# Kernel tuning notes

Measured on AMD Instinct MI355X. Metric: run time of the kernel, lower is better.

## Reference

```python
import jax, jax.numpy as jnp
import numpy as np

B, C, H, W = 16, 64, 32, 32

def conv1x1(x, w, b=None):
    # x: [b,c,h,w], w: [o,c]
    y = jnp.einsum('bchw,oc->bohw', x, w)
    return y if b is None else y + b[None, :, None, None]

def bn(x, s, b, eps=1e-5):
    # training-mode batchnorm over (N,H,W)
    m = x.mean(axis=(0, 2, 3), keepdims=True)
    v = x.var(axis=(0, 2, 3), keepdims=True)
    return (x - m) * jax.lax.rsqrt(v + eps) * s[None, :, None, None] + b[None, :, None, None]

def block(x, w1, s1, b1, w2, s2, b2, ws=None, ss=None, bs=None):
    # BasicBlock with k1=k2=1, stride 1
    y = jax.nn.relu(bn(conv1x1(x, w1), s1, b1))
    y = bn(conv1x1(y, w2), s2, b2)
    sc = x if ws is None else bn(conv1x1(x, ws), ss, bs)
    return jax.nn.relu(y + sc)

def setup_inputs():
    key = jax.random.key(0)
    ks = iter(jax.random.split(key, 32))
    def wmat(o, i):
        return jax.random.normal(next(ks), (o, i), jnp.float32) * 0.05
    d = {}
    d['xa'] = jax.random.normal(next(ks), (B, C, H, W), jnp.float32)
    d['xb'] = jax.random.normal(next(ks), (B, C, H, W), jnp.float32)
    for n in ['qa', 'qb', 'ka', 'kb']:
        d['w' + n] = wmat(C, C)
        d['b' + n] = jnp.zeros((C,), jnp.float32)
    for blk, cin, cout in [('a1', 2 * C, 2 * C), ('b1', 2 * C, 2 * C), ('a2', 2 * C, 4 * C), ('b2', 2 * C, 4 * C)]:
        d[blk + '_w1'] = wmat(cout, cin)
        d[blk + '_s1'] = jnp.ones((cout,), jnp.float32)
        d[blk + '_b1'] = jnp.zeros((cout,), jnp.float32)
        d[blk + '_w2'] = wmat(cout, cout)
        d[blk + '_s2'] = jnp.ones((cout,), jnp.float32)
        d[blk + '_b2'] = jnp.zeros((cout,), jnp.float32)
        if cin != cout:
            d[blk + '_ws'] = wmat(cout, cin)
            d[blk + '_ss'] = jnp.ones((cout,), jnp.float32)
            d[blk + '_bs'] = jnp.zeros((cout,), jnp.float32)
    for o in ['oa', 'ob']:
        d[o + '_w'] = wmat(C, 4 * C)
        d[o + '_s'] = jnp.ones((C,), jnp.float32)
        d[o + '_b'] = jnp.zeros((C,), jnp.float32)
    return d

def reference(xa, xb, wqa, bqa, wqb, bqb, wka, bka, wkb, bkb,
              a1_w1, a1_s1, a1_b1, a1_w2, a1_s2, a1_b2,
              b1_w1, b1_s1, b1_b1, b1_w2, b1_s2, b1_b2,
              a2_w1, a2_s1, a2_b1, a2_w2, a2_s2, a2_b2, a2_ws, a2_ss, a2_bs,
              b2_w1, b2_s1, b2_b1, b2_w2, b2_s2, b2_b2, b2_ws, b2_ss, b2_bs,
              oa_w, oa_s, oa_b, ob_w, ob_s, ob_b):
    b, c = xa.shape[0], xa.shape[1]
    qa = conv1x1(xa, wqa, bqa).reshape(b, c, -1)   # [b,c,na]
    qb = conv1x1(xb, wqb, bqb).reshape(b, c, -1)   # [b,c,nb]
    energy = jnp.einsum('bci,bcj->bij', qa, qb)    # [b,na,nb]
    flat = energy.reshape(b, -1)
    m = jnp.max(flat, axis=-1, keepdims=True)
    # DANet-style: softmax over the FULL flattened na*nb axis of (max - energy)
    att = jax.nn.softmax(m - flat, axis=-1).reshape(energy.shape)
    ka = conv1x1(xa, wka, bka).reshape(b, c, -1)
    kb = conv1x1(xb, wkb, bkb).reshape(b, c, -1)
    xb_att = jnp.einsum('bij,bcj->bci', att, kb).reshape(xa.shape)
    xa_att = jnp.einsum('bij,bci->bcj', att, ka).reshape(xb.shape)
    ya = jnp.concatenate([xa, xb_att], axis=1)
    yb = jnp.concatenate([xb, xa_att], axis=1)
    ya = block(ya, a1_w1, a1_s1, a1_b1, a1_w2, a1_s2, a1_b2)
    ya = block(ya, a2_w1, a2_s1, a2_b1, a2_w2, a2_s2, a2_b2, a2_ws, a2_ss, a2_bs)
    yb = block(yb, b1_w1, b1_s1, b1_b1, b1_w2, b1_s2, b1_b2)
    yb = block(yb, b2_w1, b2_s1, b2_b1, b2_w2, b2_s2, b2_b2, b2_ws, b2_ss, b2_bs)
    ya = bn(conv1x1(ya, oa_w), oa_s, oa_b)
    yb = bn(conv1x1(yb, ob_w), ob_s, ob_b)
    return (ya, yb)
```

## Files before the change

### kernel.cpp

```cpp
#include <hip/hip_runtime.h>
#include <hip/hip_bf16.h>
#include <cstddef>

static constexpr int BATCH = 16;
static constexpr int NCOPY = 16;
static constexpr int SSTR  = NCOPY * 512;

typedef __attribute__((ext_vector_type(8))) short bf16x8;
typedef __attribute__((ext_vector_type(4))) float f32x4;

__device__ __forceinline__ unsigned short f2bf(float f) {
  unsigned u = __float_as_uint(f);
  return (unsigned short)((u + 0x7fffu + ((u >> 16) & 1u)) >> 16);
}

#define SEL4(dst, arr, idx)                                   \
  do {                                                        \
    if ((idx) == 0) dst = arr[0];                             \
    else if ((idx) == 1) dst = arr[1];                        \
    else if ((idx) == 2) dst = arr[2];                        \
    else dst = arr[3];                                        \
  } while (0)

__global__ void init_kernel(float* __restrict__ t, int n) {
  int i = blockIdx.x * 256 + threadIdx.x;
  if (i < n) t[i] = 0.f;
}

struct WcvtArgs { const float* p[12]; int sz[12]; int off[12]; };
__global__ __launch_bounds__(256)
void wcvt_kernel(WcvtArgs a, unsigned short* __restrict__ dst) {
  const int t = blockIdx.x;
  const float* src = a.p[t];
  unsigned short* d = dst + a.off[t];
  const int sz = a.sz[t];
  for (int i = blockIdx.y * 256 + threadIdx.x; i < sz; i += 16 * 256)
    d[i] = f2bf(src[i]);
}

struct QKArgs { const float* X[4]; const float* W[4]; const float* B[4];
                unsigned short* Y[4]; };
__global__ __launch_bounds__(256)
void conv_qk_all_kernel(QKArgs a) {
  __shared__ float wsT[64][4];
  const int tid = threadIdx.x;
  const int z = blockIdx.z;
  const int which = z >> 4;
  const int b = z & 15;
  const int o0 = blockIdx.x << 2;
  const int px = (blockIdx.y << 9) + (tid << 1);
  const float* W; const float* X; const float* bias; unsigned short* Y;
  SEL4(W, a.W, which); SEL4(X, a.X, which); SEL4(bias, a.B, which); SEL4(Y, a.Y, which);
  {
    int c = tid >> 2, k = tid & 3;
    wsT[c][k] = W[((o0 + k) << 6) + c];
  }
  __syncthreads();
  float acc[4][2] = {};
  const float* xb = X + ((size_t)b << 16) + px;
#pragma unroll 4
  for (int c = 0; c < 64; ++c) {
    float2 xv = *reinterpret_cast<const float2*>(xb + (c << 10));
    float4 w = *reinterpret_cast<const float4*>(wsT[c]);
    acc[0][0] = fmaf(w.x, xv.x, acc[0][0]); acc[0][1] = fmaf(w.x, xv.y, acc[0][1]);
    acc[1][0] = fmaf(w.y, xv.x, acc[1][0]); acc[1][1] = fmaf(w.y, xv.y, acc[1][1]);
    acc[2][0] = fmaf(w.z, xv.x, acc[2][0]); acc[2][1] = fmaf(w.z, xv.y, acc[2][1]);
    acc[3][0] = fmaf(w.w, xv.x, acc[3][0]); acc[3][1] = fmaf(w.w, xv.y, acc[3][1]);
  }
  float b0 = bias[o0], b1 = bias[o0 + 1], b2 = bias[o0 + 2], b3 = bias[o0 + 3];
  if (which < 2) {
    ushort4 v0, v1;
    v0.x = f2bf(acc[0][0] + b0); v0.y = f2bf(acc[1][0] + b1);
    v0.z = f2bf(acc[2][0] + b2); v0.w = f2bf(acc[3][0] + b3);
    v1.x = f2bf(acc[0][1] + b0); v1.y = f2bf(acc[1][1] + b1);
    v1.z = f2bf(acc[2][1] + b2); v1.w = f2bf(acc[3][1] + b3);
    unsigned short* yt = Y + ((size_t)b << 16) + ((size_t)px << 6) + o0;
    *reinterpret_cast<ushort4*>(yt) = v0;
    *reinterpret_cast<ushort4*>(yt + 64) = v1;
  } else {
    float bv[4] = {b0, b1, b2, b3};
#pragma unroll
    for (int k = 0; k < 4; ++k) {
      ushort2 v;
      v.x = f2bf(acc[k][0] + bv[k]); v.y = f2bf(acc[k][1] + bv[k]);
      *reinterpret_cast<ushort2*>(Y + ((size_t)b << 16) + ((size_t)(o0 + k) << 10) + px) = v;
    }
  }
}

__global__ __launch_bounds__(256)
void attn_mfma_kernel(const unsigned short* __restrict__ QAt,
                      const unsigned short* __restrict__ QBt,
                      const unsigned short* __restrict__ KAc,
                      const unsigned short* __restrict__ KBc,
                      float* __restrict__ PART, float* __restrict__ bsum) {
  __shared__ __align__(16) unsigned short Ua[4096];
  __shared__ __align__(16) unsigned short Vb[4096];
  __shared__ __align__(16) unsigned short Pl[4096];
  __shared__ float red[256];
  const int tid = threadIdx.x;
  const int lane = tid & 63, w = tid >> 6;
  const int g = lane >> 4, m = lane & 15;
  const int z = blockIdx.z;
  const bool isPV = (z < 16);
  const int b = z & 15;
  const size_t nb = (size_t)b << 16;
  const size_t M1 = (size_t)1 << 20;

  if (isPV) {
    const int i0 = blockIdx.x << 6;
    const int jbase = blockIdx.y << 9;
    {
      const unsigned short* src = QAt + nb + ((size_t)i0 << 6);
#pragma unroll
      for (int s = 0; s < 2; ++s) {
        int idx = tid + (s << 8);
        int n = idx >> 3, cc = idx & 7;
        bf16x8 v = *reinterpret_cast<const bf16x8*>(src + (n << 6) + ((cc ^ (n & 7)) << 3));
        *reinterpret_cast<bf16x8*>(Ua + (idx << 3)) = v;
      }
    }
    f32x4 accO[4];
#pragma unroll
    for (int n = 0; n < 4; ++n) accO[n] = (f32x4){0.f, 0.f, 0.f, 0.f};
    float psum = 0.f;
    for (int jt = 0; jt < 8; ++jt) {
      const int j0 = jbase + (jt << 6);
      __syncthreads();
      {
        const unsigned short* src = QBt + nb + ((size_t)j0 << 6);
#pragma unroll
        for (int s = 0; s < 2; ++s) {
          int idx = tid + (s << 8);
          int n = idx >> 3, cc = idx & 7;
          bf16x8 v = *reinterpret_cast<const bf16x8*>(src + (n << 6) + ((cc ^ (n & 7)) << 3));
          *reinterpret_cast<bf16x8*>(Vb + (idx << 3)) = v;
        }
      }
      __syncthreads();
      const int jrow = (w << 4) | m;
      bf16x8 a0 = *reinterpret_cast<const bf16x8*>(Vb + (jrow << 6) + ((g ^ (jrow & 7)) << 3));
      bf16x8 a1 = *reinterpret_cast<const bf16x8*>(Vb + (jrow << 6) + (((g + 4) ^ (jrow & 7)) << 3));
      f32x4 e[4];
#pragma unroll
      for (int n = 0; n < 4; ++n) {
        const int irow = (n << 4) | m;
        bf16x8 b0v = *reinterpret_cast<const bf16x8*>(Ua + (irow << 6) + ((g ^ (irow & 7)) << 3));
        bf16x8 b1v = *reinterpret_cast<const bf16x8*>(Ua + (irow << 6) + (((g + 4) ^ (irow & 7)) << 3));
        e[n] = (f32x4){0.f, 0.f, 0.f, 0.f};
        e[n] = __builtin_amdgcn_mfma_f32_16x16x32_bf16(a0, b0v, e[n], 0, 0, 0);
        e[n] = __builtin_amdgcn_mfma_f32_16x16x32_bf16(a1, b1v, e[n], 0, 0, 0);
      }
      const int j = (w << 4) | (g << 2);
#pragma unroll
      for (int n = 0; n < 4; ++n) {
        const int irow = (n << 4) | m;
        float p0 = __expf(-e[n][0]), p1 = __expf(-e[n][1]);
        float p2 = __expf(-e[n][2]), p3 = __expf(-e[n][3]);
        psum += (p0 + p1) + (p2 + p3);
        unsigned pk01 = (unsigned)f2bf(p0) | ((unsigned)f2bf(p1) << 16);
        unsigned pk23 = (unsigned)f2bf(p2) | ((unsigned)f2bf(p3) << 16);
        int base = irow << 6;
        int off0 = base + ((((j) >> 3) ^ (irow & 7)) << 3) + (j & 7);
        int off2 = base + ((((j + 2) >> 3) ^ (irow & 7)) << 3) + ((j + 2) & 7);
        *reinterpret_cast<unsigned*>(Pl + off0) = pk01;
        *reinterpret_cast<unsigned*>(Pl + off2) = pk23;
      }
      const int crow = (w << 4) | m;
      const unsigned short* kbp = KBc + nb + ((size_t)crow << 10) + j0 + (g << 3);
      bf16x8 ka0 = *reinterpret_cast<const bf16x8*>(kbp);
      bf16x8 ka1 = *reinterpret_cast<const bf16x8*>(kbp + 32);
      __syncthreads();
#pragma unroll
      for (int n = 0; n < 4; ++n) {
        const int irow = (n << 4) | m;
        bf16x8 p0 = *reinterpret_cast<const bf16x8*>(Pl + (irow << 6) + ((g ^ (irow & 7)) << 3));
        bf16x8 p1 = *reinterpret_cast<const bf16x8*>(Pl + (irow << 6) + (((g + 4) ^ (irow & 7)) << 3));
        accO[n] = __builtin_amdgcn_mfma_f32_16x16x32_bf16(ka0, p0, accO[n], 0, 0, 0);
        accO[n] = __builtin_amdgcn_mfma_f32_16x16x32_bf16(ka1, p1, accO[n], 0, 0, 0);
      }
    }
    float* OUT = PART + ((size_t)blockIdx.y * M1) + ((size_t)(b * 64) << 10);
#pragma unroll
    for (int n = 0; n < 4; ++n) {
      const int ig = i0 + (n << 4) + m;
      const int c = (w << 4) + (g << 2);
#pragma unroll
      for (int r = 0; r < 4; ++r)
        OUT[((size_t)(c + r) << 10) + ig] = accO[n][r];
    }
    red[tid] = psum; __syncthreads();
    for (int s = 128; s > 0; s >>= 1) {
      if (tid < s) red[tid] += red[tid + s];
      __syncthreads();
    }
    if (tid == 0) atomicAdd(bsum + b, red[0]);
  } else {
    const int j0 = blockIdx.x << 6;
    const int ibase = blockIdx.y << 9;
    {
      const unsigned short* src = QBt + nb + ((size_t)j0 << 6);
#pragma unroll
      for (int s = 0; s < 2; ++s) {
        int idx = tid + (s << 8);
        int n = idx >> 3, cc = idx & 7;
        bf16x8 v = *reinterpret_cast<const bf16x8*>(src + (n << 6) + ((cc ^ (n & 7)) << 3));
        *reinterpret_cast<bf16x8*>(Ua + (idx << 3)) = v;
      }
    }
    f32x4 accO[4];
#pragma unroll
    for (int n = 0; n < 4; ++n) accO[n] = (f32x4){0.f, 0.f, 0.f, 0.f};
    for (int it = 0; it < 8; ++it) {
      const int i0 = ibase + (it << 6);
      __syncthreads();
      {
        const unsigned short* src = QAt + nb + ((size_t)i0 << 6);
#pragma unroll
        for (int s = 0; s < 2; ++s) {
          int idx = tid + (s << 8);
          int n = idx >> 3, cc = idx & 7;
          bf16x8 v = *reinterpret_cast<const bf16x8*>(src + (n << 6) + ((cc ^ (n & 7)) << 3));
          *reinterpret_cast<bf16x8*>(Vb + (idx << 3)) = v;
        }
      }
      __syncthreads();
      const int irow_a = (w << 4) | m;
      bf16x8 a0 = *reinterpret_cast<const bf16x8*>(Vb + (irow_a << 6) + ((g ^ (irow_a & 7)) << 3));
      bf16x8 a1 = *reinterpret_cast<const bf16x8*>(Vb + (irow_a << 6) + (((g + 4) ^ (irow_a & 7)) << 3));
      f32x4 e[4];
#pragma unroll
      for (int n = 0; n < 4; ++n) {
        const int jrow = (n << 4) | m;
        bf16x8 b0v = *reinterpret_cast<const bf16x8*>(Ua + (jrow << 6) + ((g ^ (jrow & 7)) << 3));
        bf16x8 b1v = *reinterpret_cast<const bf16x8*>(Ua + (jrow << 6) + (((g + 4) ^ (jrow & 7)) << 3));
        e[n] = (f32x4){0.f, 0.f, 0.f, 0.f};
        e[n] = __builtin_amdgcn_mfma_f32_16x16x32_bf16(a0, b0v, e[n], 0, 0, 0);
        e[n] = __builtin_amdgcn_mfma_f32_16x16x32_bf16(a1, b1v, e[n], 0, 0, 0);
      }
      const int i = (w << 4) | (g << 2);
#pragma unroll
      for (int n = 0; n < 4; ++n) {
        const int jrow = (n << 4) | m;
        float p0 = __expf(-e[n][0]), p1 = __expf(-e[n][1]);
        float p2 = __expf(-e[n][2]), p3 = __expf(-e[n][3]);
        unsigned pk01 = (unsigned)f2bf(p0) | ((unsigned)f2bf(p1) << 16);
        unsigned pk23 = (unsigned)f2bf(p2) | ((unsigned)f2bf(p3) << 16);
        int base = jrow << 6;
        int off0 = base + ((((i) >> 3) ^ (jrow & 7)) << 3) + (i & 7);
        int off2 = base + ((((i + 2) >> 3) ^ (jrow & 7)) << 3) + ((i + 2) & 7);
        *reinterpret_cast<unsigned*>(Pl + off0) = pk01;
        *reinterpret_cast<unsigned*>(Pl + off2) = pk23;
      }
      const int crow = (w << 4) | m;
      const unsigned short* kap = KAc + nb + ((size_t)crow << 10) + i0 + (g << 3);
      bf16x8 ka0 = *reinterpret_cast<const bf16x8*>(kap);
      bf16x8 ka1 = *reinterpret_cast<const bf16x8*>(kap + 32);
      __syncthreads();
#pragma unroll
      for (int n = 0; n < 4; ++n) {
        const int jrow = (n << 4) | m;
        bf16x8 p0 = *reinterpret_cast<const bf16x8*>(Pl + (jrow << 6) + ((g ^ (jrow & 7)) << 3));
        bf16x8 p1 = *reinterpret_cast<const bf16x8*>(Pl + (jrow << 6) + (((g + 4) ^ (jrow & 7)) << 3));
        accO[n] = __builtin_amdgcn_mfma_f32_16x16x32_bf16(ka0, p0, accO[n], 0, 0, 0);
        accO[n] = __builtin_amdgcn_mfma_f32_16x16x32_bf16(ka1, p1, accO[n], 0, 0, 0);
      }
    }
    float* OUT = PART + 2 * M1 + ((size_t)blockIdx.y * M1) + ((size_t)(b * 64) << 10);
#pragma unroll
    for (int n = 0; n < 4; ++n) {
      const int jg = j0 + (n << 4) + m;
      const int c = (w << 4) + (g << 2);
#pragma unroll
      for (int r = 0; r < 4; ++r)
        OUT[((size_t)(c + r) << 10) + jg] = accO[n][r];
    }
  }
}

__global__ __launch_bounds__(256)
void merge_kernel(const float* __restrict__ PARTb, const float* __restrict__ XA,
                  const float* __restrict__ XB, unsigned short* __restrict__ Y0b,
                  const float* __restrict__ bsum) {
  __shared__ float ts[128][66];
  const int tid = threadIdx.x;
  const int n0 = blockIdx.x << 6;
  const int b = blockIdx.y;
  const int z = blockIdx.z;
  const float invS = 1.f / bsum[b];
  const size_t M1 = (size_t)1 << 20;
  const float* XR = z ? XB : XA;
  const float* PART = PARTb + (size_t)z * 2 * M1;
  unsigned short* Y0 = Y0b + (size_t)z * 2 * M1;
#pragma unroll
  for (int it = 0; it < 4; ++it) {
    int idx = it * 256 + tid;
    int c = idx >> 4, nq = (idx & 15) << 2;
    float4 v = *reinterpret_cast<const float4*>(XR + ((size_t)(b * 64 + c) << 10) + n0 + nq);
    ts[c][nq] = v.x; ts[c][nq + 1] = v.y; ts[c][nq + 2] = v.z; ts[c][nq + 3] = v.w;
  }
#pragma unroll
  for (int it = 0; it < 4; ++it) {
    int idx = it * 256 + tid;
    int c = idx >> 4, nq = (idx & 15) << 2;
    const float* p = PART + ((size_t)(b * 64 + c) << 10) + n0 + nq;
    float4 av = *reinterpret_cast<const float4*>(p);
    float4 b4 = *reinterpret_cast<const float4*>(p + M1);
    ts[64 + c][nq]     = (av.x + b4.x) * invS;
    ts[64 + c][nq + 1] = (av.y + b4.y) * invS;
    ts[64 + c][nq + 2] = (av.z + b4.z) * invS;
    ts[64 + c][nq + 3] = (av.w + b4.w) * invS;
  }
  __syncthreads();
  const int n = tid >> 2, c0 = (tid & 3) << 5;
  unsigned short* dst = Y0 + ((size_t)(b * 1024 + n0 + n) << 7) + c0;
#pragma unroll
  for (int q8 = 0; q8 < 4; ++q8) {
    const int cb = c0 + (q8 << 3);
    unsigned w0 = (unsigned)f2bf(ts[cb + 0][n]) | ((unsigned)f2bf(ts[cb + 1][n]) << 16);
    unsigned w1 = (unsigned)f2bf(ts[cb + 2][n]) | ((unsigned)f2bf(ts[cb + 3][n]) << 16);
    unsigned w2 = (unsigned)f2bf(ts[cb + 4][n]) | ((unsigned)f2bf(ts[cb + 5][n]) << 16);
    unsigned w3 = (unsigned)f2bf(ts[cb + 6][n]) | ((unsigned)f2bf(ts[cb + 7][n]) << 16);
    *reinterpret_cast<uint4*>(dst + (q8 << 3)) = make_uint4(w0, w1, w2, w3);
  }
}

struct GBArgs { const float* g0[4]; const float* b0[4];
                const float* g1[4]; const float* b1[4]; };

template<int CIN, int OC, int SMODE, int XDIV>
__global__ __launch_bounds__(256, 4)
void conv_mfma_kernel(const unsigned short* __restrict__ T0,
                      const unsigned short* __restrict__ S0,
                      const unsigned short* __restrict__ W0,
                      unsigned short* __restrict__ Yout0,
                      const float* __restrict__ sums0A, long s0str,
                      const float* __restrict__ sums1A, long s1str,
                      GBArgs gb,
                      float* __restrict__ outSums0,
                      int COUT, long tstr, long sstr, long wstr, long ystr) {
  constexpr int KS = CIN / 32;
  constexpr int ROWB = CIN * 2;
  constexpr int CPR = CIN / 8;
  __shared__ __align__(16) unsigned char Xs[64 * ROWB];
  __shared__ float scs[(SMODE >= 1) ? CIN : 1];
  __shared__ float shs[(SMODE >= 1) ? CIN : 1];
  __shared__ float sc2[(SMODE == 3) ? CIN : 1];
  __shared__ float sh2[(SMODE == 3) ? CIN : 1];
  const int tid = threadIdx.x;
  const int lane = tid & 63, w = tid >> 6;
  const int g = lane >> 4, m = lane & 15;
  const int z = blockIdx.z;
  const int zi = z >> XDIV;
  const int obase = blockIdx.x * (OC << 6) + (w << 4);
  const int nbase = blockIdx.y << 6;
  const unsigned short* Tin = T0 + (size_t)zi * tstr;
  const unsigned short* Sin = (SMODE >= 2) ? (S0 + (size_t)zi * sstr) : nullptr;
  const unsigned short* Wb  = W0 + (size_t)z * wstr;
  unsigned short* Yout      = Yout0 + (size_t)z * ystr;
  float* outSums            = outSums0 + (size_t)z * SSTR;
  if (SMODE >= 1) {
    const float* s0 = sums0A + (size_t)zi * s0str;
    const float* gg0; const float* bb0;
    SEL4(gg0, gb.g0, zi); SEL4(bb0, gb.b0, zi);
    const float invN = 1.f / 16384.f;
    for (int c = tid; c < CIN; c += 256) {
      float ss = 0.f, qq = 0.f;
#pragma unroll
      for (int p = 0; p < NCOPY; ++p) {
        ss += s0[p * 512 + c];
        qq += s0[p * 512 + 256 + c];
      }
      float mm = ss * invN;
      float vv = qq * invN - mm * mm;
      float s = gg0[c] * rsqrtf(vv + 1e-5f);
      scs[c] = s; shs[c] = bb0[c] - mm * s;
    }
    if (SMODE == 3) {
      const float* s1 = sums1A + (size_t)zi * s1str;
      const float* gg1; const float* bb1;
      SEL4(gg1, gb.g1, zi); SEL4(bb1, gb.b1, zi);
      for (int c = tid; c < CIN; c += 256) {
        float ss = 0.f, qq = 0.f;
#pragma unroll
        for (int p = 0; p < NCOPY; ++p) {
          ss += s1[p * 512 + c];
          qq += s1[p * 512 + 256 + c];
        }
        float mm = ss * invN;
        float vv = qq * invN - mm * mm;
        float s = gg1[c] * rsqrtf(vv + 1e-5f);
        sc2[c] = s; sh2[c] = bb1[c] - mm * s;
      }
    }
    __syncthreads();
  }
#pragma unroll
  for (int it = 0; it < (64 * CPR) / 256; ++it) {
    const int idx = it * 256 + tid;
    const int row = idx / CPR;
    const int cc = idx % CPR;
    bf16x8 v = *reinterpret_cast<const bf16x8*>(
        Tin + (size_t)(nbase + row) * CIN + cc * 8);
    if (SMODE >= 1) {
      bf16x8 sv;
      if (SMODE >= 2)
        sv = *reinterpret_cast<const bf16x8*>(
            Sin + (size_t)(nbase + row) * CIN + cc * 8);
      const int c0 = cc * 8;
#pragma unroll
      for (int j = 0; j < 8; ++j) {
        float x = __uint_as_float((unsigned)(unsigned short)v[j] << 16);
        x = fmaf(x, scs[c0 + j], shs[c0 + j]);
        if (SMODE == 2)
          x += __uint_as_float((unsigned)(unsigned short)sv[j] << 16);
        if (SMODE == 3) {
          float y = __uint_as_float((unsigned)(unsigned short)sv[j] << 16);
          x += fmaf(y, sc2[c0 + j], sh2[c0 + j]);
        }
        x = fmaxf(x, 0.f);
        v[j] = (short)f2bf(x);
      }
    }
    const int byte = (cc << 4) ^ ((row & 7) << 4);
    *reinterpret_cast<bf16x8*>(Xs + row * ROWB + byte) = v;
  }
  __syncthreads();
  bf16x8 af[KS][OC];
#pragma unroll
  for (int oc = 0; oc < OC; ++oc) {
    const unsigned short* Wr = Wb + (size_t)(obase + (oc << 6) + m) * CIN + (g << 3);
#pragma unroll
    for (int k = 0; k < KS; ++k)
      af[k][oc] = *reinterpret_cast<const bf16x8*>(Wr + (k << 5));
  }
  float sr[OC][4], qr[OC][4];
#pragma unroll
  for (int oc = 0; oc < OC; ++oc)
#pragma unroll
    for (int r = 0; r < 4; ++r) { sr[oc][r] = 0.f; qr[oc][r] = 0.f; }
#pragma unroll
  for (int nt = 0; nt < 4; ++nt) {
    const int row = (nt << 4) + m;
    const unsigned char* lrow = Xs + row * ROWB;
    const int swz = (row & 7) << 4;
    f32x4 acc[OC];
#pragma unroll
    for (int oc = 0; oc < OC; ++oc) acc[oc] = (f32x4){0.f, 0.f, 0.f, 0.f};
#pragma unroll
    for (int k = 0; k < KS; ++k) {
      const int byte = ((k << 6) + (g << 4)) ^ swz;
      bf16x8 bv = *reinterpret_cast<const bf16x8*>(lrow + byte);
#pragma unroll
      for (int oc = 0; oc < OC; ++oc)
        acc[oc] = __builtin_amdgcn_mfma_f32_16x16x32_bf16(af[k][oc], bv, acc[oc], 0, 0, 0);
    }
#pragma unroll
    for (int oc = 0; oc < OC; ++oc) {
      ushort4 v;
      v.x = f2bf(acc[oc][0]); v.y = f2bf(acc[oc][1]);
      v.z = f2bf(acc[oc][2]); v.w = f2bf(acc[oc][3]);
      *reinterpret_cast<ushort4*>(
          Yout + (size_t)(nbase + row) * COUT + obase + (oc << 6) + (g << 2)) = v;
#pragma unroll
      for (int r = 0; r < 4; ++r) {
        sr[oc][r] += acc[oc][r];
        qr[oc][r] = fmaf(acc[oc][r], acc[oc][r], qr[oc][r]);
      }
    }
  }
#pragma unroll
  for (int oc = 0; oc < OC; ++oc)
#pragma unroll
    for (int r = 0; r < 4; ++r) {
      for (int off = 1; off < 16; off <<= 1) {
        sr[oc][r] += __shfl_xor(sr[oc][r], off);
        qr[oc][r] += __shfl_xor(qr[oc][r], off);
      }
    }
  if (m == 0) {
    float* dst = outSums + (blockIdx.y & (NCOPY - 1)) * 512;
#pragma unroll
    for (int oc = 0; oc < OC; ++oc)
#pragma unroll
      for (int r = 0; r < 4; ++r) {
        atomicAdd(&dst[obase + (oc << 6) + (g << 2) + r], sr[oc][r]);
        atomicAdd(&dst[256 + obase + (oc << 6) + (g << 2) + r], qr[oc][r]);
      }
  }
}

__global__ __launch_bounds__(256)
void writeout_t_kernel(const unsigned short* __restrict__ F0,
                       const float* __restrict__ sumsA,
                       GBArgs gb,
                       float* __restrict__ out0) {
  __shared__ float ts[64][66];
  __shared__ float sc[64], sh[64];
  const int tid = threadIdx.x;
  const int z = blockIdx.z;
  const size_t M1 = (size_t)1 << 20;
  const unsigned short* F = F0 + (size_t)z * M1;
  float* outp = out0 + (size_t)z * M1;
  if (tid < 64) {
    const float* sums = sumsA + (size_t)z * SSTR;
    const float* gg; const float* bb;
    SEL4(gg, gb.g0, z); SEL4(bb, gb.b0, z);
    float s0 = 0.f, q0 = 0.f;
#pragma unroll
    for (int p = 0; p < NCOPY; ++p) {
      s0 += sums[p * 512 + tid];
      q0 += sums[p * 512 + 256 + tid];
    }
    const float invN = 1.f / 16384.f;
    float mm = s0 * invN;
    float vv = q0 * invN - mm * mm;
    float s = gg[tid] * rsqrtf(vv + 1e-5f);
    sc[tid] = s; sh[tid] = bb[tid] - mm * s;
  }
  __syncthreads();
  const int n0 = blockIdx.x << 6;
  const int b = blockIdx.y;
  {
    const int n = tid >> 2, c0 = (tid & 3) << 4;
    const unsigned short* Fr = F + ((size_t)(b * 1024 + n0 + n) << 6) + c0;
    uint4 v0 = *reinterpret_cast<const uint4*>(Fr);
    uint4 v1 = *reinterpret_cast<const uint4*>(Fr + 8);
    unsigned vw[8] = {v0.x, v0.y, v0.z, v0.w, v1.x, v1.y, v1.z, v1.w};
#pragma unroll
    for (int jw = 0; jw < 8; ++jw) {
      int c = c0 + jw * 2;
      float x0 = __uint_as_float((vw[jw] & 0xffffu) << 16);
      float x1 = __uint_as_float((vw[jw] >> 16) << 16);
      ts[c][n] = fmaf(x0, sc[c], sh[c]);
      ts[c + 1][n] = fmaf(x1, sc[c + 1], sh[c + 1]);
    }
  }
  __syncthreads();
  const int c = tid >> 2, nq = (tid & 3) << 4;
  float* orow = outp + ((size_t)(b * 64 + c) << 10) + n0 + nq;
#pragma unroll
  for (int q = 0; q < 4; ++q) {
    float4 ov;
    ov.x = ts[c][nq + q * 4 + 0]; ov.y = ts[c][nq + q * 4 + 1];
    ov.z = ts[c][nq + q * 4 + 2]; ov.w = ts[c][nq + q * 4 + 3];
    *reinterpret_cast<float4*>(orow + q * 4) = ov;
  }
}

extern "C" void kernel_launch(void* const* d_in, const int* in_sizes, int n_in,
                              void* d_out, int out_size, void* d_ws, size_t ws_size,
                              hipStream_t stream) {
  float* wsf = (float*)d_ws;
  const size_t M1 = (size_t)1 << 20;
  const size_t H1 = (size_t)1 << 19;

  unsigned short* QAt = (unsigned short*)wsf;
  unsigned short* QBt = (unsigned short*)(wsf + H1);
  unsigned short* KAc = (unsigned short*)(wsf + 2 * H1);
  unsigned short* KBc = (unsigned short*)(wsf + 3 * H1);
  float* PART1 = wsf + 2 * M1;
  unsigned short* Y0A = (unsigned short*)(wsf + 10 * M1);
  unsigned short* T1a = (unsigned short*)(wsf + 12 * M1);
  unsigned short* T2a = (unsigned short*)(wsf + 14 * M1);
  unsigned short* T3a = (unsigned short*)(wsf + 18 * M1);
  unsigned short* T4a = (unsigned short*)(wsf + 26 * M1);
  unsigned short* Fba = (unsigned short*)(wsf + 30 * M1);
  float* tail = wsf + 31 * M1;
  float* bsum = tail;
  float* stats = tail + 16;
  unsigned short* wbf = (unsigned short*)(stats + 12 * SSTR);

  const float* pp[46];
  for (int i = 0; i < 46 && i < n_in; ++i) pp[i] = (const float*)d_in[i];

  const int initN = 16 + 12 * SSTR;
  init_kernel<<<(initN + 255) / 256, 256, 0, stream>>>(tail, initN);

  const int widx[12] = {10, 16, 13, 19, 22, 28, 31, 37, 25, 34, 40, 43};
  WcvtArgs wa;
  int woff[12];
  {
    int run = 0;
    for (int i = 0; i < 12; ++i) {
      wa.p[i] = pp[widx[i]];
      wa.sz[i] = in_sizes[widx[i]];
      wa.off[i] = run; woff[i] = run;
      run += in_sizes[widx[i]];
    }
  }
  wcvt_kernel<<<dim3(12, 16), 256, 0, stream>>>(wa, wbf);

  QKArgs qk;
  qk.X[0] = pp[0]; qk.W[0] = pp[2]; qk.B[0] = pp[3]; qk.Y[0] = QAt;
  qk.X[1] = pp[1]; qk.W[1] = pp[4]; qk.B[1] = pp[5]; qk.Y[1] = QBt;
  qk.X[2] = pp[0]; qk.W[2] = pp[6]; qk.B[2] = pp[7]; qk.Y[2] = KAc;
  qk.X[3] = pp[1]; qk.W[3] = pp[8]; qk.B[3] = pp[9]; qk.Y[3] = KBc;
  conv_qk_all_kernel<<<dim3(16, 2, 64), 256, 0, stream>>>(qk);

  attn_mfma_kernel<<<dim3(16, 2, 32), 256, 0, stream>>>(
      QAt, QBt, KAc, KBc, PART1, bsum);
  merge_kernel<<<dim3(16, BATCH, 2), 256, 0, stream>>>(PART1, pp[0], pp[1], Y0A, bsum);

  float* S_c1 = stats;
  float* S_c2 = stats + 2 * SSTR;
  float* S_q  = stats + 4 * SSTR;
  float* S_c4 = stats + 8 * SSTR;
  float* S_c6 = stats + 10 * SSTR;

  const long SH1 = (long)2 * M1;
  const long SH2 = (long)4 * M1;
  GBArgs gbE = {};
  GBArgs gb;

  conv_mfma_kernel<128, 2, 0, 0><<<dim3(1, 256, 2), 256, 0, stream>>>(
      Y0A, nullptr, wbf + woff[0], T1a, nullptr, 0, nullptr, 0, gbE,
      S_c1, 128, SH1, 0, 16384, SH1);

  gb = gbE;
  gb.g0[0] = pp[11]; gb.b0[0] = pp[12]; gb.g0[1] = pp[17]; gb.b0[1] = pp[18];
  conv_mfma_kernel<128, 2, 1, 0><<<dim3(1, 256, 2), 256, 0, stream>>>(
      T1a, nullptr, wbf + woff[2], T2a, S_c1, SSTR, nullptr, 0, gb,
      S_c2, 128, SH1, 0, 16384, SH1);

  gb = gbE;
  gb.g0[0] = pp[14]; gb.b0[0] = pp[15]; gb.g0[1] = pp[20]; gb.b0[1] = pp[21];
  conv_mfma_kernel<128, 2, 2, 1><<<dim3(2, 256, 4), 256, 0, stream>>>(
      T2a, Y0A, wbf + woff[4], T3a, S_c2, SSTR, nullptr, 0, gb,
      S_q, 256, SH1, SH1, 32768, SH2);

  gb = gbE;
  gb.g0[0] = pp[23]; gb.b0[0] = pp[24]; gb.g0[1] = pp[32]; gb.b0[1] = pp[33];
  conv_mfma_kernel<256, 2, 1, 0><<<dim3(2, 256, 2), 256, 0, stream>>>(
      T3a, nullptr, wbf + woff[8], T4a, S_q, 2 * SSTR, nullptr, 0, gb,
      S_c4, 256, (long)8 * M1, 0, 65536, SH2);

  gb = gbE;
  gb.g0[0] = pp[26]; gb.b0[0] = pp[27]; gb.g0[1] = pp[35]; gb.b0[1] = pp[36];
  gb.g1[0] = pp[29]; gb.b1[0] = pp[30]; gb.g1[1] = pp[38]; gb.b1[1] = pp[39];
  conv_mfma_kernel<256, 1, 3, 0><<<dim3(1, 256, 2), 256, 0, stream>>>(
      T4a, T3a + SH2 , wbf + woff[10], Fba, S_c4, SSTR,
      S_q + SSTR, 2 * SSTR, gb,
      S_c6, 64, SH2, (long)8 * M1, 16384, (long)M1);

  gb = gbE;
  gb.g0[0] = pp[41]; gb.b0[0] = pp[42]; gb.g0[1] = pp[44]; gb.b0[1] = pp[45];
  writeout_t_kernel<<<dim3(16, BATCH, 2), 256, 0, stream>>>(
      Fba, S_c6, gb, (float*)d_out);
}
```

Baseline: 167.0 us.

## Compute Q/K 1x1 projections with bf16 MFMA after transposing inputs to channel-last

```diff
diff --git a/kernel.cpp b/kernel.cpp
--- a/kernel.cpp
+++ b/kernel.cpp
@@ -27,7 +27,7 @@
   if (i < n) t[i] = 0.f;
 }
 
-struct WcvtArgs { const float* p[12]; int sz[12]; int off[12]; };
+struct WcvtArgs { const float* p[16]; int sz[16]; int off[16]; };
 __global__ __launch_bounds__(256)
 void wcvt_kernel(WcvtArgs a, unsigned short* __restrict__ dst) {
   const int t = blockIdx.x;
@@ -38,52 +38,102 @@
     d[i] = f2bf(src[i]);
 }
 
-struct QKArgs { const float* X[4]; const float* W[4]; const float* B[4];
-                unsigned short* Y[4]; };
 __global__ __launch_bounds__(256)
-void conv_qk_all_kernel(QKArgs a) {
-  __shared__ float wsT[64][4];
+void xcvt_kernel(const float* __restrict__ XA, const float* __restrict__ XB,
+                 unsigned short* __restrict__ XAt, unsigned short* __restrict__ XBt) {
+  __shared__ float ts[64][66];
   const int tid = threadIdx.x;
+  const int n0 = blockIdx.x << 6;
+  const int b = blockIdx.y;
   const int z = blockIdx.z;
+  const float* X = z ? XB : XA;
+  unsigned short* XT = z ? XBt : XAt;
+#pragma unroll
+  for (int it = 0; it < 4; ++it) {
+    int idx = it * 256 + tid;
+    int c = idx >> 4, nq = (idx & 15) << 2;
+    float4 v = *reinterpret_cast<const float4*>(X + ((size_t)(b * 64 + c) << 10) + n0 + nq);
+    ts[c][nq] = v.x; ts[c][nq + 1] = v.y; ts[c][nq + 2] = v.z; ts[c][nq + 3] = v.w;
+  }
+  __syncthreads();
+  const int n = tid >> 2, c0 = (tid & 3) << 4;
+  unsigned short* dst = XT + ((size_t)(b * 1024 + n0 + n) << 6) + c0;
+  unsigned w0 = (unsigned)f2bf(ts[c0 + 0][n]) | ((unsigned)f2bf(ts[c0 + 1][n]) << 16);
+  unsigned w1 = (unsigned)f2bf(ts[c0 + 2][n]) | ((unsigned)f2bf(ts[c0 + 3][n]) << 16);
+  unsigned w2 = (unsigned)f2bf(ts[c0 + 4][n]) | ((unsigned)f2bf(ts[c0 + 5][n]) << 16);
+  unsigned w3 = (unsigned)f2bf(ts[c0 + 6][n]) | ((unsigned)f2bf(ts[c0 + 7][n]) << 16);
+  unsigned w4 = (unsigned)f2bf(ts[c0 + 8][n]) | ((unsigned)f2bf(ts[c0 + 9][n]) << 16);
+  unsigned w5 = (unsigned)f2bf(ts[c0 + 10][n]) | ((unsigned)f2bf(ts[c0 + 11][n]) << 16);
+  unsigned w6 = (unsigned)f2bf(ts[c0 + 12][n]) | ((unsigned)f2bf(ts[c0 + 13][n]) << 16);
+  unsigned w7 = (unsigned)f2bf(ts[c0 + 14][n]) | ((unsigned)f2bf(ts[c0 + 15][n]) << 16);
+  *reinterpret_cast<uint4*>(dst) = make_uint4(w0, w1, w2, w3);
+  *reinterpret_cast<uint4*>(dst + 8) = make_uint4(w4, w5, w6, w7);
+}
+
+struct QBias { const float* p[4]; };
+__global__ __launch_bounds__(256, 4)
+void qk_mfma_kernel(const unsigned short* __restrict__ XAt,
+                    const unsigned short* __restrict__ XBt,
+                    const unsigned short* __restrict__ wq,
+                    QBias qb,
+                    unsigned short* __restrict__ QAt, unsigned short* __restrict__ QBt,
+                    unsigned short* __restrict__ KAc, unsigned short* __restrict__ KBc) {
+  __shared__ __align__(16) unsigned char Xs[64 * 128];
+  const int tid = threadIdx.x;
+  const int lane = tid & 63, w = tid >> 6;
+  const int g = lane >> 4, m = lane & 15;
+  const int nbase = blockIdx.x << 6;
+  const int z = blockIdx.y;
   const int which = z >> 4;
   const int b = z & 15;
-  const int o0 = blockIdx.x << 2;
-  const int px = (blockIdx.y << 9) + (tid << 1);
-  const float* W; const float* X; const float* bias; unsigned short* Y;
-  SEL4(W, a.W, which); SEL4(X, a.X, which); SEL4(bias, a.B, which); SEL4(Y, a.Y, which);
-  {
-    int c = tid >> 2, k = tid & 3;
-    wsT[c][k] = W[((o0 + k) << 6) + c];
+  const unsigned short* XT = (which & 1) ? XBt : XAt;
+  const unsigned short* Wb = wq + which * 4096;
+  const float* bias;
+  SEL4(bias, qb.p, which);
+#pragma unroll
+  for (int it = 0; it < 2; ++it) {
+    int idx = it * 256 + tid;
+    int row = idx >> 3, cc = idx & 7;
+    bf16x8 v = *reinterpret_cast<const bf16x8*>(
+        XT + ((size_t)(b * 1024 + nbase + row) << 6) + cc * 8);
+    const int byte = (cc << 4) ^ ((row & 7) << 4);
+    *reinterpret_cast<bf16x8*>(Xs + row * 128 + byte) = v;
   }
   __syncthreads();
-  float acc[4][2] = {};
-  const float* xb = X + ((size_t)b << 16) + px;
-#pragma unroll 4
-  for (int c = 0; c < 64; ++c) {
-    float2 xv = *reinterpret_cast<const float2*>(xb + (c << 10));
-    float4 w = *reinterpret_cast<const float4*>(wsT[c]);
-    acc[0][0] = fmaf(w.x, xv.x, acc[0][0]); acc[0][1] = fmaf(w.x, xv.y, acc[0][1]);
-    acc[1][0] = fmaf(w.y, xv.x, acc[1][0]); acc[1][1] = fmaf(w.y, xv.y, acc[1][1]);
-    acc[2][0] = fmaf(w.z, xv.x, acc[2][0]); acc[2][1] = fmaf(w.z, xv.y, acc[2][1]);
-    acc[3][0] = fmaf(w.w, xv.x, acc[3][0]); acc[3][1] = fmaf(w.w, xv.y, acc[3][1]);
-  }
-  float b0 = bias[o0], b1 = bias[o0 + 1], b2 = bias[o0 + 2], b3 = bias[o0 + 3];
-  if (which < 2) {
-    ushort4 v0, v1;
-    v0.x = f2bf(acc[0][0] + b0); v0.y = f2bf(acc[1][0] + b1);
-    v0.z = f2bf(acc[2][0] + b2); v0.w = f2bf(acc[3][0] + b3);
-    v1.x = f2bf(acc[0][1] + b0); v1.y = f2bf(acc[1][1] + b1);
-    v1.z = f2bf(acc[2][1] + b2); v1.w = f2bf(acc[3][1] + b3);
-    unsigned short* yt = Y + ((size_t)b << 16) + ((size_t)px << 6) + o0;
-    *reinterpret_cast<ushort4*>(yt) = v0;
-    *reinterpret_cast<ushort4*>(yt + 64) = v1;
-  } else {
-    float bv[4] = {b0, b1, b2, b3};
-#pragma unroll
-    for (int k = 0; k < 4; ++k) {
-      ushort2 v;
-      v.x = f2bf(acc[k][0] + bv[k]); v.y = f2bf(acc[k][1] + bv[k]);
-      *reinterpret_cast<ushort2*>(Y + ((size_t)b << 16) + ((size_t)(o0 + k) << 10) + px) = v;
+  const int o0 = w << 4;
+  const unsigned short* Wr = Wb + (size_t)(o0 + m) * 64 + (g << 3);
+  bf16x8 af0 = *reinterpret_cast<const bf16x8*>(Wr);
+  bf16x8 af1 = *reinterpret_cast<const bf16x8*>(Wr + 32);
+  float bv[4];
+#pragma unroll
+  for (int r = 0; r < 4; ++r) bv[r] = bias[o0 + (g << 2) + r];
+#pragma unroll
+  for (int nt = 0; nt < 4; ++nt) {
+    const int row = (nt << 4) + m;
+    const unsigned char* lrow = Xs + row * 128;
+    const int swz = (row & 7) << 4;
+    f32x4 acc = (f32x4){0.f, 0.f, 0.f, 0.f};
+    {
+      bf16x8 b0 = *reinterpret_cast<const bf16x8*>(lrow + ((g << 4) ^ swz));
+      acc = __builtin_amdgcn_mfma_f32_16x16x32_bf16(af0, b0, acc, 0, 0, 0);
+      bf16x8 b1 = *reinterpret_cast<const bf16x8*>(lrow + ((64 + (g << 4)) ^ swz));
+      acc = __builtin_amdgcn_mfma_f32_16x16x32_bf16(af1, b1, acc, 0, 0, 0);
+    }
+#pragma unroll
+    for (int r = 0; r < 4; ++r) acc[r] += bv[r];
+    if (which < 2) {
+      unsigned short* Yq = (which == 0) ? QAt : QBt;
+      ushort4 v;
+      v.x = f2bf(acc[0]); v.y = f2bf(acc[1]);
+      v.z = f2bf(acc[2]); v.w = f2bf(acc[3]);
+      *reinterpret_cast<ushort4*>(
+          Yq + ((size_t)(b * 1024 + nbase + row) << 6) + o0 + (g << 2)) = v;
+    } else {
+      unsigned short* Kc = (which == 2) ? KAc : KBc;
+#pragma unroll
+      for (int r = 0; r < 4; ++r)
+        Kc[((size_t)b << 16) + ((size_t)(o0 + (g << 2) + r) << 10) + nbase + row] =
+            f2bf(acc[r]);
     }
   }
 }
@@ -560,6 +610,8 @@
   unsigned short* KAc = (unsigned short*)(wsf + 2 * H1);
   unsigned short* KBc = (unsigned short*)(wsf + 3 * H1);
   float* PART1 = wsf + 2 * M1;
+  unsigned short* XAt = (unsigned short*)(wsf + 6 * M1);
+  unsigned short* XBt = (unsigned short*)(wsf + 7 * M1);
   unsigned short* Y0A = (unsigned short*)(wsf + 10 * M1);
   unsigned short* T1a = (unsigned short*)(wsf + 12 * M1);
   unsigned short* T2a = (unsigned short*)(wsf + 14 * M1);
@@ -577,26 +629,27 @@
   const int initN = 16 + 12 * SSTR;
   init_kernel<<<(initN + 255) / 256, 256, 0, stream>>>(tail, initN);
 
-  const int widx[12] = {10, 16, 13, 19, 22, 28, 31, 37, 25, 34, 40, 43};
+  const int widx[16] = {2, 4, 6, 8,
+                        10, 16, 13, 19, 22, 28, 31, 37, 25, 34, 40, 43};
   WcvtArgs wa;
-  int woff[12];
+  int woff[16];
   {
     int run = 0;
-    for (int i = 0; i < 12; ++i) {
+    for (int i = 0; i < 16; ++i) {
       wa.p[i] = pp[widx[i]];
       wa.sz[i] = in_sizes[widx[i]];
       wa.off[i] = run; woff[i] = run;
       run += in_sizes[widx[i]];
     }
   }
-  wcvt_kernel<<<dim3(12, 16), 256, 0, stream>>>(wa, wbf);
-
-  QKArgs qk;
-  qk.X[0] = pp[0]; qk.W[0] = pp[2]; qk.B[0] = pp[3]; qk.Y[0] = QAt;
-  qk.X[1] = pp[1]; qk.W[1] = pp[4]; qk.B[1] = pp[5]; qk.Y[1] = QBt;
-  qk.X[2] = pp[0]; qk.W[2] = pp[6]; qk.B[2] = pp[7]; qk.Y[2] = KAc;
-  qk.X[3] = pp[1]; qk.W[3] = pp[8]; qk.B[3] = pp[9]; qk.Y[3] = KBc;
-  conv_qk_all_kernel<<<dim3(16, 2, 64), 256, 0, stream>>>(qk);
+  wcvt_kernel<<<dim3(16, 16), 256, 0, stream>>>(wa, wbf);
+
+  xcvt_kernel<<<dim3(16, BATCH, 2), 256, 0, stream>>>(pp[0], pp[1], XAt, XBt);
+
+  QBias qb;
+  qb.p[0] = pp[3]; qb.p[1] = pp[5]; qb.p[2] = pp[7]; qb.p[3] = pp[9];
+  qk_mfma_kernel<<<dim3(16, 64), 256, 0, stream>>>(
+      XAt, XBt, wbf + woff[0], qb, QAt, QBt, KAc, KBc);
 
   attn_mfma_kernel<<<dim3(16, 2, 32), 256, 0, stream>>>(
       QAt, QBt, KAc, KBc, PART1, bsum);
@@ -614,32 +667,32 @@
   GBArgs gb;
 
   conv_mfma_kernel<128, 2, 0, 0><<<dim3(1, 256, 2), 256, 0, stream>>>(
-      Y0A, nullptr, wbf + woff[0], T1a, nullptr, 0, nullptr, 0, gbE,
+      Y0A, nullptr, wbf + woff[4], T1a, nullptr, 0, nullptr, 0, gbE,
       S_c1, 128, SH1, 0, 16384, SH1);
 
   gb = gbE;
   gb.g0[0] = pp[11]; gb.b0[0] = pp[12]; gb.g0[1] = pp[17]; gb.b0[1] = pp[18];
   conv_mfma_kernel<128, 2, 1, 0><<<dim3(1, 256, 2), 256, 0, stream>>>(
-      T1a, nullptr, wbf + woff[2], T2a, S_c1, SSTR, nullptr, 0, gb,
+      T1a, nullptr, wbf + woff[6], T2a, S_c1, SSTR, nullptr, 0, gb,
       S_c2, 128, SH1, 0, 16384, SH1);
 
   gb = gbE;
   gb.g0[0] = pp[14]; gb.b0[0] = pp[15]; gb.g0[1] = pp[20]; gb.b0[1] = pp[21];
   conv_mfma_kernel<128, 2, 2, 1><<<dim3(2, 256, 4), 256, 0, stream>>>(
-      T2a, Y0A, wbf + woff[4], T3a, S_c2, SSTR, nullptr, 0, gb,
+      T2a, Y0A, wbf + woff[8], T3a, S_c2, SSTR, nullptr, 0, gb,
       S_q, 256, SH1, SH1, 32768, SH2);
 
   gb = gbE;
   gb.g0[0] = pp[23]; gb.b0[0] = pp[24]; gb.g0[1] = pp[32]; gb.b0[1] = pp[33];
   conv_mfma_kernel<256, 2, 1, 0><<<dim3(2, 256, 2), 256, 0, stream>>>(
-      T3a, nullptr, wbf + woff[8], T4a, S_q, 2 * SSTR, nullptr, 0, gb,
+      T3a, nullptr, wbf + woff[12], T4a, S_q, 2 * SSTR, nullptr, 0, gb,
       S_c4, 256, (long)8 * M1, 0, 65536, SH2);
 
   gb = gbE;
   gb.g0[0] = pp[26]; gb.b0[0] = pp[27]; gb.g0[1] = pp[35]; gb.b0[1] = pp[36];
   gb.g1[0] = pp[29]; gb.b1[0] = pp[30]; gb.g1[1] = pp[38]; gb.b1[1] = pp[39];
   conv_mfma_kernel<256, 1, 3, 0><<<dim3(1, 256, 2), 256, 0, stream>>>(
-      T4a, T3a + SH2 , wbf + woff[10], Fba, S_c4, SSTR,
+      T4a, T3a + SH2 , wbf + woff[14], Fba, S_c4, SSTR,
       S_q + SSTR, 2 * SSTR, gb,
       S_c6, 64, SH2, (long)8 * M1, 16384, (long)M1);
 
```

Measured after the change: 148.6 us. 11.0% less time.
